# Kernel optimization log

Hardware: AMD Instinct MI355X
Metric: run time of the kernel (lower is better)

## Reference

```python
import jax, jax.numpy as jnp
import numpy as np

B, H, W, C = 4, 64, 64, 1280
NH = 16          # num heads
HD = C // NH     # 80 features per head
WS = 14          # window size
REL = 2 * WS - 1 # 27 relative-position entries per axis
EPS = 1e-6


def setup_inputs() -> dict:
    key = jax.random.key(0)
    ks = jax.random.split(key, 16)
    s = 0.02
    return {
        "imagelike_bhwc": jax.random.normal(ks[0], (B, H, W, C), jnp.float32),
        "ln1_g": jnp.ones((C,), jnp.float32),
        "ln1_b": jnp.zeros((C,), jnp.float32),
        "qkv_w": jax.random.normal(ks[1], (C, 3 * C), jnp.float32) * s,
        "qkv_b": jnp.zeros((3 * C,), jnp.float32),
        "proj_w": jax.random.normal(ks[2], (C, C), jnp.float32) * s,
        "proj_b": jnp.zeros((C,), jnp.float32),
        "rel_pos_h": jax.random.normal(ks[3], (REL, HD), jnp.float32) * s,
        "rel_pos_w": jax.random.normal(ks[4], (REL, HD), jnp.float32) * s,
        "ln2_g": jnp.ones((C,), jnp.float32),
        "ln2_b": jnp.zeros((C,), jnp.float32),
        "mlp_w1": jax.random.normal(ks[5], (C, 4 * C), jnp.float32) * s,
        "mlp_b1": jnp.zeros((4 * C,), jnp.float32),
        "mlp_w2": jax.random.normal(ks[6], (4 * C, C), jnp.float32) * s,
        "mlp_b2": jnp.zeros((C,), jnp.float32),
    }


def _layernorm(t, g, b):
    mu = jnp.mean(t, axis=-1, keepdims=True)
    var = jnp.var(t, axis=-1, keepdims=True)
    return (t - mu) * jax.lax.rsqrt(var + EPS) * g + b


def reference(imagelike_bhwc, ln1_g, ln1_b, qkv_w, qkv_b, proj_w, proj_b,
              rel_pos_h, rel_pos_w, ln2_g, ln2_b, mlp_w1, mlp_b1, mlp_w2, mlp_b2):
    x = imagelike_bhwc
    b, h, w, c = x.shape
    hd = c // NH
    scale = hd ** -0.5
    # --- image -> windows (pad to multiple of WS) ---
    hp, wp = (-h) % WS, (-w) % WS
    xp = jnp.pad(x, ((0, 0), (0, hp), (0, wp), (0, 0)))
    Hp, Wp = h + hp, w + wp
    ny, nx = Hp // WS, Wp // WS
    win = xp.reshape(b, ny, WS, nx, WS, c).transpose(0, 1, 3, 2, 4, 5)
    win = win.reshape(b * ny * nx, WS, WS, c)      # (Bw, S, S, C)
    Bw, N = win.shape[0], WS * WS
    # --- pre-attention layernorm + qkv ---
    t = _layernorm(win, ln1_g, ln1_b)
    qkv = t.reshape(Bw, N, c) @ qkv_w + qkv_b      # (Bw, N, 3C)
    qkv = qkv.reshape(Bw, N, 3, NH, hd).transpose(2, 0, 3, 1, 4)  # (3,Bw,NH,N,hd)
    q, k, v = qkv[0], qkv[1], qkv[2]
    # --- scores + decomposed relative position bias ---
    attn = jnp.einsum('bhqd,bhkd->bhqk', q * scale, k)            # (Bw,NH,N,N)
    idx = jnp.arange(WS)[:, None] - jnp.arange(WS)[None, :] + (WS - 1)
    Rh = rel_pos_h[idx]                                           # (WS,WS,hd)
    Rw = rel_pos_w[idx]                                           # (WS,WS,hd)
    qr = q.reshape(Bw, NH, WS, WS, hd)
    bias_h = jnp.einsum('bnyxd,ykd->bnyxk', qr, Rh)               # (Bw,NH,WS,WS,WS)
    bias_w = jnp.einsum('bnyxd,xkd->bnyxk', qr, Rw)
    bias = (bias_h[..., :, None] + bias_w[..., None, :]).reshape(Bw, NH, N, N)
    attn = jax.nn.softmax(attn + bias, axis=-1)
    out = jnp.einsum('bhqk,bhkd->bhqd', attn, v)                  # (Bw,NH,N,hd)
    out = out.transpose(0, 2, 1, 3).reshape(Bw, WS, WS, c)
    out = out @ proj_w + proj_b
    attn_out = out + win                                          # residual 1
    # --- MLP ---
    t2 = _layernorm(attn_out, ln2_g, ln2_b)
    mlp = jax.nn.gelu(t2 @ mlp_w1 + mlp_b1, approximate=False) @ mlp_w2 + mlp_b2
    out = mlp + attn_out                                          # residual 2
    # --- windows -> image (remove padding) ---
    img = out.reshape(b, ny, nx, WS, WS, c).transpose(0, 1, 3, 2, 4, 5)
    img = img.reshape(b, Hp, Wp, c)
    return img[:, :h, :w, :]
```

## Files before the change

### kernel.cpp

```cpp
#include <hip/hip_runtime.h>

typedef __attribute__((ext_vector_type(8))) short short8;
typedef __attribute__((ext_vector_type(4))) float f32x4;

#define GLBP(p) ((const __attribute__((address_space(1))) void*)(p))
#define LDSP(p) ((__attribute__((address_space(3))) void*)(p))

__device__ __forceinline__ float bf2f(unsigned short u) {
  return __uint_as_float(((unsigned int)u) << 16);
}
__device__ __forceinline__ unsigned short f2bf(float f) {
  unsigned int u = __float_as_uint(f);
  u += 0x7fff + ((u >> 16) & 1);
  return (unsigned short)(u >> 16);
}

__device__ __forceinline__ void tok2pix(int gt, int& b, int& py, int& px) {
  int w = gt / 196, t = gt - w * 196;
  b = w / 25;
  int wr = w - b * 25;
  int wy = wr / 5, wx = wr - wy * 5;
  int ty = t / 14;
  py = wy * 14 + ty;
  px = wx * 14 + (t - ty * 14);
}

__global__ void k_transpose(const float* __restrict__ W, unsigned short* __restrict__ Wt,
                            int K, int N) {
  __shared__ float tile[32][33];
  int tx = threadIdx.x, ty = threadIdx.y;
  int n0 = blockIdx.x * 32, k0 = blockIdx.y * 32;
#pragma unroll
  for (int i = 0; i < 4; ++i)
    tile[ty + 8 * i][tx] = W[(size_t)(k0 + ty + 8 * i) * N + n0 + tx];
  __syncthreads();
#pragma unroll
  for (int i = 0; i < 4; ++i)
    Wt[(size_t)(n0 + ty + 8 * i) * K + k0 + tx] = f2bf(tile[tx][ty + 8 * i]);
}

__global__ __launch_bounds__(256) void k_ln1(const float* __restrict__ x,
                                             const float* __restrict__ g,
                                             const float* __restrict__ be,
                                             unsigned short* __restrict__ A1,
                                             int w0, int ctok) {
  int m = blockIdx.x, tid = threadIdx.x;
  int b, py, px;
  tok2pix(w0 * 196 + m, b, py, px);
  bool valid = (m < ctok) && (py < 64) && (px < 64);
  const float* row = x + ((size_t)((b * 64 + py) * 64 + px)) * 1280;
  float v[5];
#pragma unroll
  for (int i = 0; i < 5; ++i) v[i] = valid ? row[tid + 256 * i] : 0.f;
  float s = 0.f, ss = 0.f;
#pragma unroll
  for (int i = 0; i < 5; ++i) { s += v[i]; ss += v[i] * v[i]; }
#pragma unroll
  for (int o = 32; o > 0; o >>= 1) { s += __shfl_down(s, o); ss += __shfl_down(ss, o); }
  __shared__ float rs[8];
  int wid = tid >> 6, lane = tid & 63;
  if (lane == 0) { rs[wid] = s; rs[wid + 4] = ss; }
  __syncthreads();
  s = rs[0] + rs[1] + rs[2] + rs[3];
  ss = rs[4] + rs[5] + rs[6] + rs[7];
  float mu = s * (1.f / 1280.f);
  float var = ss * (1.f / 1280.f) - mu * mu;
  float rinv = rsqrtf(var + 1e-6f);
  unsigned short* o1 = A1 + (size_t)m * 1280;
#pragma unroll
  for (int i = 0; i < 5; ++i) {
    int c = tid + 256 * i;
    o1[c] = f2bf((v[i] - mu) * rinv * g[c] + be[c]);
  }
}

__global__ __launch_bounds__(256) void k_ln2(const unsigned short* __restrict__ AT,
                                             const float* __restrict__ g,
                                             const float* __restrict__ be,
                                             unsigned short* __restrict__ A2) {
  int m = blockIdx.x, tid = threadIdx.x;
  const unsigned short* row = AT + (size_t)m * 1280;
  float v[5];
#pragma unroll
  for (int i = 0; i < 5; ++i) v[i] = bf2f(row[tid + 256 * i]);
  float s = 0.f, ss = 0.f;
#pragma unroll
  for (int i = 0; i < 5; ++i) { s += v[i]; ss += v[i] * v[i]; }
#pragma unroll
  for (int o = 32; o > 0; o >>= 1) { s += __shfl_down(s, o); ss += __shfl_down(ss, o); }
  __shared__ float rs[8];
  int wid = tid >> 6, lane = tid & 63;
  if (lane == 0) { rs[wid] = s; rs[wid + 4] = ss; }
  __syncthreads();
  s = rs[0] + rs[1] + rs[2] + rs[3];
  ss = rs[4] + rs[5] + rs[6] + rs[7];
  float mu = s * (1.f / 1280.f);
  float var = ss * (1.f / 1280.f) - mu * mu;
  float rinv = rsqrtf(var + 1e-6f);
  unsigned short* o1 = A2 + (size_t)m * 1280;
#pragma unroll
  for (int i = 0; i < 5; ++i) {
    int c = tid + 256 * i;
    o1[c] = f2bf((v[i] - mu) * rinv * g[c] + be[c]);
  }
}

template <int EPI>
__global__ __launch_bounds__(512, 2) void k_gemm256(const unsigned short* __restrict__ A,
                                                    const unsigned short* __restrict__ Bt,
                                                    int K, int N, int gx,
                                                    const float* __restrict__ bias,
                                                    void* __restrict__ outp,
                                                    const float* __restrict__ xres,
                                                    const unsigned short* __restrict__ attnres,
                                                    int w0, int ctok) {
  __shared__ __align__(16) char smem[131072];
  int tid = threadIdx.x;
  int w = tid >> 6, lane = tid & 63;
  int nwg = gridDim.x, bid = blockIdx.x;
  int q = nwg >> 3, r = nwg & 7;
  int xcd = bid & 7, loc = bid >> 3;
  int wg = (xcd < r ? xcd * (q + 1) : r * (q + 1) + (xcd - r) * q) + loc;
  int bx = wg % gx, by = wg / gx;
  int mBase = by * 256, nBase = bx * 256;
  int wr = w >> 2, wc = w & 3;
  int la = lane & 15, lg = lane >> 4;

  int rS = w * 16 + (lane >> 2);
  int kbyte = (((lane & 3) ^ ((lane >> 3) & 3)) << 4);
  const char* Ab = (const char*)A;
  const char* Bb = (const char*)Bt;
  const char* pa0 = Ab + ((size_t)(mBase + rS) * K) * 2 + kbyte;
  const char* pa1 = Ab + ((size_t)(mBase + 128 + rS) * K) * 2 + kbyte;
  const char* pb0 = Bb + ((size_t)(nBase + rS) * K) * 2 + kbyte;
  const char* pb1 = Bb + ((size_t)(nBase + 128 + rS) * K) * 2 + kbyte;
  int ldsw = w * 1024;

  auto STAGE = [&](int t) {
    int b = (t & 3) * 32768;
    size_t ko = (size_t)t * 64;
    __builtin_amdgcn_global_load_lds(GLBP(pa0 + ko), LDSP(smem + b + ldsw), 16, 0, 0);
    __builtin_amdgcn_global_load_lds(GLBP(pa1 + ko), LDSP(smem + b + 8192 + ldsw), 16, 0, 0);
    __builtin_amdgcn_global_load_lds(GLBP(pb0 + ko), LDSP(smem + b + 16384 + ldsw), 16, 0, 0);
    __builtin_amdgcn_global_load_lds(GLBP(pb1 + ko), LDSP(smem + b + 24576 + ldsw), 16, 0, 0);
  };

  int swz = ((lg ^ ((la >> 1) & 3)) << 4);
  int offA[8], offB[4];
#pragma unroll
  for (int m = 0; m < 8; ++m) offA[m] = (wr * 128 + m * 16 + la) * 64 + swz;
#pragma unroll
  for (int n = 0; n < 4; ++n) offB[n] = (wc * 64 + n * 16 + la) * 64 + swz;

  const f32x4 z4 = {0.f, 0.f, 0.f, 0.f};
  f32x4 acc[8][4];
#pragma unroll
  for (int m = 0; m < 8; ++m)
#pragma unroll
    for (int n = 0; n < 4; ++n) acc[m][n] = z4;

  int NT = K >> 5;
  STAGE(0);
  STAGE(1);
  STAGE(2);
  for (int t = 0; t < NT; ++t) {
    if (t + 2 < NT)
      asm volatile("s_waitcnt vmcnt(8)" ::: "memory");
    else if (t + 1 < NT)
      asm volatile("s_waitcnt vmcnt(4)" ::: "memory");
    else
      asm volatile("s_waitcnt vmcnt(0)" ::: "memory");
    __builtin_amdgcn_s_barrier();
    __builtin_amdgcn_sched_barrier(0);
    if (t + 3 < NT) STAGE(t + 3);
    const char* buf = (const char*)smem + (t & 3) * 32768;
    short8 af[8], bfr[4];
#pragma unroll
    for (int m = 0; m < 8; ++m) af[m] = *(const short8*)(buf + offA[m]);
#pragma unroll
    for (int n = 0; n < 4; ++n) bfr[n] = *(const short8*)(buf + 16384 + offB[n]);
    __builtin_amdgcn_s_setprio(1);
#pragma unroll
    for (int m = 0; m < 8; ++m)
#pragma unroll
      for (int n = 0; n < 4; ++n)
        acc[m][n] = __builtin_amdgcn_mfma_f32_16x16x32_bf16(af[m], bfr[n], acc[m][n], 0, 0, 0);
    __builtin_amdgcn_s_setprio(0);
  }

#pragma unroll
  for (int m = 0; m < 8; ++m) {
#pragma unroll
    for (int n = 0; n < 4; ++n) {
      int col = nBase + wc * 64 + n * 16 + la;
      float bcol = bias[col];
#pragma unroll
      for (int j = 0; j < 4; ++j) {
        int row = mBase + wr * 128 + m * 16 + lg * 4 + j;
        float v = acc[m][n][j] + bcol;
        if (EPI == 0) {
          ((unsigned short*)outp)[(size_t)row * N + col] = f2bf(v);
        } else if (EPI == 2) {
          float gg = 0.5f * v * (1.f + erff(v * 0.70710678118654752f));
          ((unsigned short*)outp)[(size_t)row * N + col] = f2bf(gg);
        } else if (EPI == 1) {
          if (row < ctok) {
            int b, py, px;
            tok2pix(w0 * 196 + row, b, py, px);
            float wv = (py < 64 && px < 64)
                           ? xres[((size_t)((b * 64 + py) * 64 + px)) * 1280 + col]
                           : 0.f;
            ((unsigned short*)outp)[(size_t)row * 1280 + col] = f2bf(v + wv);
          }
        } else {
          if (row < ctok) {
            int b, py, px;
            tok2pix(w0 * 196 + row, b, py, px);
            if (py < 64 && px < 64)
              ((float*)outp)[((size_t)((b * 64 + py) * 64 + px)) * 1280 + col] =
                  v + bf2f(attnres[(size_t)row * 1280 + col]);
          }
        }
      }
    }
  }
}

__global__ __launch_bounds__(256) void k_relbias(const unsigned short* __restrict__ qkv,
                                                 const float* __restrict__ rph,
                                                 const float* __restrict__ rpw,
                                                 float* __restrict__ B) {
  int wh = blockIdx.x;
  int w = wh >> 4, nh = wh & 15;
  const unsigned short* qb = qkv + (size_t)w * 196 * 3840 + nh * 80;
  for (int id = threadIdx.x; id < 196 * 28; id += 256) {
    int t = id / 28, which = id - t * 28;
    int y = t / 14, xx = t - y * 14;
    const float* R = (which < 14) ? (rph + (size_t)(y - which + 13) * 80)
                                  : (rpw + (size_t)(xx - (which - 14) + 13) * 80);
    const unsigned short* q = qb + (size_t)t * 3840;
    float acc = 0.f;
#pragma unroll
    for (int d8 = 0; d8 < 10; ++d8) {
      short8 qv = *(const short8*)(q + d8 * 8);
      const float4* Rv = (const float4*)(R + d8 * 8);
      float4 ra = Rv[0], rb = Rv[1];
      acc += bf2f((unsigned short)qv[0]) * ra.x + bf2f((unsigned short)qv[1]) * ra.y +
             bf2f((unsigned short)qv[2]) * ra.z + bf2f((unsigned short)qv[3]) * ra.w +
             bf2f((unsigned short)qv[4]) * rb.x + bf2f((unsigned short)qv[5]) * rb.y +
             bf2f((unsigned short)qv[6]) * rb.z + bf2f((unsigned short)qv[7]) * rb.w;
    }
    B[(size_t)wh * (196 * 28) + id] = acc;
  }
}

__global__ __launch_bounds__(256) void k_attn(const unsigned short* __restrict__ qkv,
                                              const float* __restrict__ Bias,
                                              unsigned short* __restrict__ AO) {
  __shared__ unsigned short Qs[208 * 96];
  __shared__ unsigned short Ks[208 * 96];
  __shared__ unsigned short Vt[80 * 224];
  __shared__ unsigned short Ps[4][16 * 224];
  int wh = blockIdx.x;
  int w = wh >> 4, nh = wh & 15;
  int tid = threadIdx.x, wid = tid >> 6, lane = tid & 63;
  const unsigned short* base = qkv + (size_t)w * 196 * 3840 + nh * 80;
  short8 z8 = {0, 0, 0, 0, 0, 0, 0, 0};
  for (int c = tid; c < 208 * 12; c += 256) {
    int t = c / 12, d8 = (c - t * 12) * 8;
    short8 qv = z8, kv = z8;
    if (t < 196 && d8 < 80) {
      const unsigned short* p = base + (size_t)t * 3840 + d8;
      qv = *(const short8*)(p);
      kv = *(const short8*)(p + 1280);
    }
    *(short8*)(Qs + t * 96 + d8) = qv;
    *(short8*)(Ks + t * 96 + d8) = kv;
  }
  for (int c = tid; c < 208 * 10; c += 256) {
    int t = c / 10, d8 = (c - t * 10) * 8;
    short8 vv = z8;
    if (t < 196) vv = *(const short8*)(base + (size_t)t * 3840 + 2560 + d8);
#pragma unroll
    for (int e = 0; e < 8; ++e) Vt[(d8 + e) * 224 + t] = (unsigned short)vv[e];
  }
  for (int i = tid; i < 80 * 16; i += 256) Vt[(i >> 4) * 224 + 208 + (i & 15)] = 0;
  __syncthreads();

  int la = lane & 15, lg = lane >> 4;
  const float scale = 0.111803398874989485f;
  const f32x4 z4 = {0.f, 0.f, 0.f, 0.f};
  unsigned short* P = Ps[wid];

  for (int rb = wid; rb < 13; rb += 4) {
    f32x4 s[13];
#pragma unroll
    for (int i = 0; i < 13; ++i) s[i] = z4;
#pragma unroll
    for (int kk = 0; kk < 3; ++kk) {
      short8 a = *(const short8*)(Qs + (rb * 16 + la) * 96 + kk * 32 + lg * 8);
#pragma unroll
      for (int ni = 0; ni < 13; ++ni) {
        short8 bb = *(const short8*)(Ks + (ni * 16 + la) * 96 + kk * 32 + lg * 8);
        s[ni] = __builtin_amdgcn_mfma_f32_16x16x32_bf16(a, bb, s[ni], 0, 0, 0);
      }
    }
#pragma unroll
    for (int j = 0; j < 4; ++j) {
      int rloc = lg * 4 + j;
      int t = rb * 16 + rloc;
      float v[13];
      float mx = -3e30f;
#pragma unroll
      for (int ci = 0; ci < 13; ++ci) {
        int key = ci * 16 + la;
        float val = s[ci][j] * scale;
        if (key < 196 && t < 196) {
          const float* Bp = Bias + ((size_t)wh * 196 + t) * 28;
          int ky = key / 14, kx = key - ky * 14;
          val += Bp[ky] + Bp[14 + kx];
        }
        if (key >= 196) val = -3e30f;
        v[ci] = val;
        mx = fmaxf(mx, val);
      }
#pragma unroll
      for (int o = 1; o < 16; o <<= 1) mx = fmaxf(mx, __shfl_xor(mx, o));
      float sum = 0.f;
#pragma unroll
      for (int ci = 0; ci < 13; ++ci) {
        float e = __expf(v[ci] - mx);
        v[ci] = e;
        sum += e;
      }
#pragma unroll
      for (int o = 1; o < 16; o <<= 1) sum += __shfl_xor(sum, o);
      float inv = 1.f / sum;
#pragma unroll
      for (int ci = 0; ci < 13; ++ci) P[rloc * 224 + ci * 16 + la] = f2bf(v[ci] * inv);
      P[rloc * 224 + 208 + la] = 0;
    }
    f32x4 o5[5];
#pragma unroll
    for (int i = 0; i < 5; ++i) o5[i] = z4;
#pragma unroll
    for (int kc = 0; kc < 7; ++kc) {
      short8 a = *(const short8*)(P + la * 224 + kc * 32 + lg * 8);
#pragma unroll
      for (int ni = 0; ni < 5; ++ni) {
        short8 bb = *(const short8*)(Vt + (ni * 16 + la) * 224 + kc * 32 + lg * 8);
        o5[ni] = __builtin_amdgcn_mfma_f32_16x16x32_bf16(a, bb, o5[ni], 0, 0, 0);
      }
    }
#pragma unroll
    for (int ni = 0; ni < 5; ++ni)
#pragma unroll
      for (int j = 0; j < 4; ++j) {
        int t = rb * 16 + lg * 4 + j;
        if (t < 196)
          AO[((size_t)w * 196 + t) * 1280 + nh * 80 + ni * 16 + la] = f2bf(o5[ni][j]);
      }
  }
}

extern "C" void kernel_launch(void* const* d_in, const int* in_sizes, int n_in,
                              void* d_out, int out_size, void* d_ws, size_t ws_size,
                              hipStream_t stream) {
  const float* x = (const float*)d_in[0];
  const float* ln1g = (const float*)d_in[1];
  const float* ln1b = (const float*)d_in[2];
  const float* qkvw = (const float*)d_in[3];
  const float* qkvb = (const float*)d_in[4];
  const float* projw = (const float*)d_in[5];
  const float* projb = (const float*)d_in[6];
  const float* rph = (const float*)d_in[7];
  const float* rpw = (const float*)d_in[8];
  const float* ln2g = (const float*)d_in[9];
  const float* ln2b = (const float*)d_in[10];
  const float* w1 = (const float*)d_in[11];
  const float* b1 = (const float*)d_in[12];
  const float* w2 = (const float*)d_in[13];
  const float* b2 = (const float*)d_in[14];
  float* out = (float*)d_out;

  const size_t woff = (3840ull * 1280 + 1280ull * 1280 + 5120ull * 1280 + 1280ull * 5120) * 2;
  const int NWopts[7] = {100, 50, 25, 10, 5, 2, 1};
  int NW = 0, Mb = 0;
  for (int i = 0; i < 7; ++i) {
    int nw = NWopts[i];
    int mb = ((nw * 196 + 255) / 256) * 256;
    size_t tot = woff + (size_t)mb * 2560  + (size_t)mb * 7680  +
                 (size_t)mb * 2560  + (size_t)nw * 16 * 196 * 28 * 4  +
                 (size_t)mb * 2560 ;
    if (tot <= ws_size) { NW = nw; Mb = mb; break; }
  }
  if (!NW) return;

  char* p = (char*)d_ws;
  unsigned short* qkvwT = (unsigned short*)p; p += 3840ull * 1280 * 2;
  unsigned short* projwT = (unsigned short*)p; p += 1280ull * 1280 * 2;
  unsigned short* w1T = (unsigned short*)p; p += 5120ull * 1280 * 2;
  unsigned short* w2T = (unsigned short*)p; p += 1280ull * 5120 * 2;
  unsigned short* A1 = (unsigned short*)p; p += (size_t)Mb * 2560;
  unsigned short* QKV = (unsigned short*)p; p += (size_t)Mb * 7680;
  unsigned short* AO = (unsigned short*)p; p += (size_t)Mb * 2560;
  float* BIAS = (float*)p; p += (size_t)NW * 16 * 196 * 28 * 4;
  unsigned short* ATTN = (unsigned short*)p;
  unsigned short* Hb = QKV;
  unsigned short* A2 = A1;

  k_transpose<<<dim3(120, 40), dim3(32, 8), 0, stream>>>(qkvw, qkvwT, 1280, 3840);
  k_transpose<<<dim3(40, 40), dim3(32, 8), 0, stream>>>(projw, projwT, 1280, 1280);
  k_transpose<<<dim3(160, 40), dim3(32, 8), 0, stream>>>(w1, w1T, 1280, 5120);
  k_transpose<<<dim3(40, 160), dim3(32, 8), 0, stream>>>(w2, w2T, 5120, 1280);

  int gy = Mb / 256;
  int nchunks = (100 + NW - 1) / NW;
  for (int c = 0; c < nchunks; ++c) {
    int w0 = c * NW;
    int cw = (100 - w0 < NW) ? (100 - w0) : NW;
    int ctok = cw * 196;
    k_ln1<<<Mb, 256, 0, stream>>>(x, ln1g, ln1b, A1, w0, ctok);
    k_gemm256<0><<<15 * gy, 512, 0, stream>>>(A1, qkvwT, 1280, 3840, 15, qkvb, (void*)QKV,
                                              nullptr, nullptr, 0, 0);
    k_relbias<<<cw * 16, 256, 0, stream>>>(QKV, rph, rpw, BIAS);
    k_attn<<<cw * 16, 256, 0, stream>>>(QKV, BIAS, AO);
    k_gemm256<1><<<5 * gy, 512, 0, stream>>>(AO, projwT, 1280, 1280, 5, projb, (void*)ATTN,
                                             x, nullptr, w0, ctok);
    k_ln2<<<Mb, 256, 0, stream>>>(ATTN, ln2g, ln2b, A2);
    k_gemm256<2><<<20 * gy, 512, 0, stream>>>(A2, w1T, 1280, 5120, 20, b1, (void*)Hb,
                                              nullptr, nullptr, 0, 0);
    k_gemm256<3><<<5 * gy, 512, 0, stream>>>(Hb, w2T, 5120, 1280, 5, b2, (void*)out,
                                             nullptr, ATTN, w0, ctok);
  }
}
```

Measured before the change: 1.869 ms.

## Split GEMM inner loop into two halves and restructure attention kernel

```diff
diff --git a/kernel.cpp b/kernel.cpp
--- a/kernel.cpp
+++ b/kernel.cpp
@@ -164,24 +164,36 @@
   STAGE(1);
   STAGE(2);
   for (int t = 0; t < NT; ++t) {
-    if (t + 2 < NT)
+    int rem = NT - 1 - t;
+    if (rem >= 2)
       asm volatile("s_waitcnt vmcnt(8)" ::: "memory");
-    else if (t + 1 < NT)
+    else if (rem == 1)
       asm volatile("s_waitcnt vmcnt(4)" ::: "memory");
     else
       asm volatile("s_waitcnt vmcnt(0)" ::: "memory");
     __builtin_amdgcn_s_barrier();
     __builtin_amdgcn_sched_barrier(0);
-    if (t + 3 < NT) STAGE(t + 3);
     const char* buf = (const char*)smem + (t & 3) * 32768;
     short8 af[8], bfr[4];
 #pragma unroll
-    for (int m = 0; m < 8; ++m) af[m] = *(const short8*)(buf + offA[m]);
+    for (int m = 0; m < 4; ++m) af[m] = *(const short8*)(buf + offA[m]);
 #pragma unroll
     for (int n = 0; n < 4; ++n) bfr[n] = *(const short8*)(buf + 16384 + offB[n]);
+    if (t + 3 < NT) STAGE(t + 3);
     __builtin_amdgcn_s_setprio(1);
 #pragma unroll
-    for (int m = 0; m < 8; ++m)
+    for (int m = 0; m < 4; ++m)
+#pragma unroll
+      for (int n = 0; n < 4; ++n)
+        acc[m][n] = __builtin_amdgcn_mfma_f32_16x16x32_bf16(af[m], bfr[n], acc[m][n], 0, 0, 0);
+    __builtin_amdgcn_s_setprio(0);
+    __builtin_amdgcn_s_barrier();
+    __builtin_amdgcn_sched_barrier(0);
+#pragma unroll
+    for (int m = 4; m < 8; ++m) af[m] = *(const short8*)(buf + offA[m]);
+    __builtin_amdgcn_s_setprio(1);
+#pragma unroll
+    for (int m = 4; m < 8; ++m)
 #pragma unroll
       for (int n = 0; n < 4; ++n)
         acc[m][n] = __builtin_amdgcn_mfma_f32_16x16x32_bf16(af[m], bfr[n], acc[m][n], 0, 0, 0);
@@ -229,7 +241,7 @@
 __global__ __launch_bounds__(256) void k_relbias(const unsigned short* __restrict__ qkv,
                                                  const float* __restrict__ rph,
                                                  const float* __restrict__ rpw,
-                                                 float* __restrict__ B) {
+                                                 unsigned short* __restrict__ B) {
   int wh = blockIdx.x;
   int w = wh >> 4, nh = wh & 15;
   const unsigned short* qb = qkv + (size_t)w * 196 * 3840 + nh * 80;
@@ -250,76 +262,87 @@
              bf2f((unsigned short)qv[4]) * rb.x + bf2f((unsigned short)qv[5]) * rb.y +
              bf2f((unsigned short)qv[6]) * rb.z + bf2f((unsigned short)qv[7]) * rb.w;
     }
-    B[(size_t)wh * (196 * 28) + id] = acc;
-  }
-}
-
-__global__ __launch_bounds__(256) void k_attn(const unsigned short* __restrict__ qkv,
-                                              const float* __restrict__ Bias,
+    B[(size_t)wh * (196 * 28) + id] = f2bf(acc);
+  }
+}
+
+__global__ __launch_bounds__(512) void k_attn(const unsigned short* __restrict__ qkv,
+                                              const unsigned short* __restrict__ Bias,
                                               unsigned short* __restrict__ AO) {
-  __shared__ unsigned short Qs[208 * 96];
-  __shared__ unsigned short Ks[208 * 96];
-  __shared__ unsigned short Vt[80 * 224];
-  __shared__ unsigned short Ps[4][16 * 224];
+  __shared__ unsigned short Ks[208 * 104];
+  __shared__ unsigned short Vt[80 * 248];
+  __shared__ unsigned short Ps[8][16 * 248];
+  __shared__ unsigned short Bls[196 * 28];
   int wh = blockIdx.x;
   int w = wh >> 4, nh = wh & 15;
   int tid = threadIdx.x, wid = tid >> 6, lane = tid & 63;
+  int la = lane & 15, lg = lane >> 4;
   const unsigned short* base = qkv + (size_t)w * 196 * 3840 + nh * 80;
-  short8 z8 = {0, 0, 0, 0, 0, 0, 0, 0};
-  for (int c = tid; c < 208 * 12; c += 256) {
-    int t = c / 12, d8 = (c - t * 12) * 8;
-    short8 qv = z8, kv = z8;
-    if (t < 196 && d8 < 80) {
-      const unsigned short* p = base + (size_t)t * 3840 + d8;
-      qv = *(const short8*)(p);
-      kv = *(const short8*)(p + 1280);
-    }
-    *(short8*)(Qs + t * 96 + d8) = qv;
-    *(short8*)(Ks + t * 96 + d8) = kv;
-  }
-  for (int c = tid; c < 208 * 10; c += 256) {
-    int t = c / 10, d8 = (c - t * 10) * 8;
-    short8 vv = z8;
-    if (t < 196) vv = *(const short8*)(base + (size_t)t * 3840 + 2560 + d8);
-#pragma unroll
-    for (int e = 0; e < 8; ++e) Vt[(d8 + e) * 224 + t] = (unsigned short)vv[e];
-  }
-  for (int i = tid; i < 80 * 16; i += 256) Vt[(i >> 4) * 224 + 208 + (i & 15)] = 0;
+  const short8 z8 = {0, 0, 0, 0, 0, 0, 0, 0};
+
+  for (int c = tid; c < 208 * 13; c += 512) {
+    int t = c / 13, seg = c - t * 13;
+    short8 kv = z8;
+    if (t < 196 && seg < 10) kv = *(const short8*)(base + (size_t)t * 3840 + 1280 + seg * 8);
+    *(short8*)(Ks + t * 104 + seg * 8) = kv;
+  }
+  for (int c = tid; c < 28 * 80; c += 512) {
+    int d = c % 80, tb = c / 80;
+    short8 pk;
+#pragma unroll
+    for (int e = 0; e < 8; ++e) {
+      int t = tb * 8 + e;
+      pk[e] = (t < 196) ? (short)base[(size_t)t * 3840 + 2560 + d] : (short)0;
+    }
+    *(short8*)(Vt + d * 248 + tb * 8) = pk;
+  }
+  for (int i = tid; i < 196 * 28; i += 512) Bls[i] = Bias[(size_t)wh * (196 * 28) + i];
   __syncthreads();
 
-  int la = lane & 15, lg = lane >> 4;
+  int kyv[13], kxv[13];
+#pragma unroll
+  for (int ci = 0; ci < 13; ++ci) {
+    int key = ci * 16 + la;
+    kyv[ci] = key / 14;
+    kxv[ci] = key - kyv[ci] * 14;
+  }
+
   const float scale = 0.111803398874989485f;
   const f32x4 z4 = {0.f, 0.f, 0.f, 0.f};
   unsigned short* P = Ps[wid];
 
-  for (int rb = wid; rb < 13; rb += 4) {
+  auto process = [&](int rb) {
+    short8 qa[3];
+#pragma unroll
+    for (int kk = 0; kk < 3; ++kk) {
+      int t = rb * 16 + la;
+      int d = kk * 32 + lg * 8;
+      qa[kk] = (t < 196 && d < 80) ? *(const short8*)(base + (size_t)t * 3840 + d) : z8;
+    }
     f32x4 s[13];
 #pragma unroll
     for (int i = 0; i < 13; ++i) s[i] = z4;
 #pragma unroll
     for (int kk = 0; kk < 3; ++kk) {
-      short8 a = *(const short8*)(Qs + (rb * 16 + la) * 96 + kk * 32 + lg * 8);
 #pragma unroll
       for (int ni = 0; ni < 13; ++ni) {
-        short8 bb = *(const short8*)(Ks + (ni * 16 + la) * 96 + kk * 32 + lg * 8);
-        s[ni] = __builtin_amdgcn_mfma_f32_16x16x32_bf16(a, bb, s[ni], 0, 0, 0);
+        short8 bb = *(const short8*)(Ks + (ni * 16 + la) * 104 + kk * 32 + lg * 8);
+        s[ni] = __builtin_amdgcn_mfma_f32_16x16x32_bf16(qa[kk], bb, s[ni], 0, 0, 0);
       }
     }
 #pragma unroll
     for (int j = 0; j < 4; ++j) {
       int rloc = lg * 4 + j;
       int t = rb * 16 + rloc;
+      bool tval = t < 196;
+      const unsigned short* Bp = Bls + (tval ? t : 0) * 28;
       float v[13];
       float mx = -3e30f;
 #pragma unroll
       for (int ci = 0; ci < 13; ++ci) {
         int key = ci * 16 + la;
         float val = s[ci][j] * scale;
-        if (key < 196 && t < 196) {
-          const float* Bp = Bias + ((size_t)wh * 196 + t) * 28;
-          int ky = key / 14, kx = key - ky * 14;
-          val += Bp[ky] + Bp[14 + kx];
-        }
+        if (key < 196 && tval) val += bf2f(Bp[kyv[ci]]) + bf2f(Bp[14 + kxv[ci]]);
         if (key >= 196) val = -3e30f;
         v[ci] = val;
         mx = fmaxf(mx, val);
@@ -337,18 +360,18 @@
       for (int o = 1; o < 16; o <<= 1) sum += __shfl_xor(sum, o);
       float inv = 1.f / sum;
 #pragma unroll
-      for (int ci = 0; ci < 13; ++ci) P[rloc * 224 + ci * 16 + la] = f2bf(v[ci] * inv);
-      P[rloc * 224 + 208 + la] = 0;
+      for (int ci = 0; ci < 13; ++ci) P[rloc * 248 + ci * 16 + la] = f2bf(v[ci] * inv);
+      P[rloc * 248 + 208 + la] = 0;
     }
     f32x4 o5[5];
 #pragma unroll
     for (int i = 0; i < 5; ++i) o5[i] = z4;
 #pragma unroll
     for (int kc = 0; kc < 7; ++kc) {
-      short8 a = *(const short8*)(P + la * 224 + kc * 32 + lg * 8);
+      short8 a = *(const short8*)(P + la * 248 + kc * 32 + lg * 8);
 #pragma unroll
       for (int ni = 0; ni < 5; ++ni) {
-        short8 bb = *(const short8*)(Vt + (ni * 16 + la) * 224 + kc * 32 + lg * 8);
+        short8 bb = *(const short8*)(Vt + (ni * 16 + la) * 248 + kc * 32 + lg * 8);
         o5[ni] = __builtin_amdgcn_mfma_f32_16x16x32_bf16(a, bb, o5[ni], 0, 0, 0);
       }
     }
@@ -360,7 +383,10 @@
         if (t < 196)
           AO[((size_t)w * 196 + t) * 1280 + nh * 80 + ni * 16 + la] = f2bf(o5[ni][j]);
       }
-  }
+  };
+
+  process(wid);
+  if (wid < 5) process(wid + 8);
 }
 
 extern "C" void kernel_launch(void* const* d_in, const int* in_sizes, int n_in,
@@ -390,7 +416,7 @@
     int nw = NWopts[i];
     int mb = ((nw * 196 + 255) / 256) * 256;
     size_t tot = woff + (size_t)mb * 2560  + (size_t)mb * 7680  +
-                 (size_t)mb * 2560  + (size_t)nw * 16 * 196 * 28 * 4  +
+                 (size_t)mb * 2560  + (size_t)nw * 16 * 196 * 28 * 2  +
                  (size_t)mb * 2560 ;
     if (tot <= ws_size) { NW = nw; Mb = mb; break; }
   }
@@ -404,7 +430,7 @@
   unsigned short* A1 = (unsigned short*)p; p += (size_t)Mb * 2560;
   unsigned short* QKV = (unsigned short*)p; p += (size_t)Mb * 7680;
   unsigned short* AO = (unsigned short*)p; p += (size_t)Mb * 2560;
-  float* BIAS = (float*)p; p += (size_t)NW * 16 * 196 * 28 * 4;
+  unsigned short* BIAS = (unsigned short*)p; p += (size_t)NW * 16 * 196 * 28 * 2;
   unsigned short* ATTN = (unsigned short*)p;
   unsigned short* Hb = QKV;
   unsigned short* A2 = A1;
@@ -424,7 +450,7 @@
     k_gemm256<0><<<15 * gy, 512, 0, stream>>>(A1, qkvwT, 1280, 3840, 15, qkvb, (void*)QKV,
                                               nullptr, nullptr, 0, 0);
     k_relbias<<<cw * 16, 256, 0, stream>>>(QKV, rph, rpw, BIAS);
-    k_attn<<<cw * 16, 256, 0, stream>>>(QKV, BIAS, AO);
+    k_attn<<<cw * 16, 512, 0, stream>>>(QKV, BIAS, AO);
     k_gemm256<1><<<5 * gy, 512, 0, stream>>>(AO, projwT, 1280, 1280, 5, projb, (void*)ATTN,
                                              x, nullptr, w0, ctok);
     k_ln2<<<Mb, 256, 0, stream>>>(ATTN, ln2g, ln2b, A2);
```

Result: faster. 1.730 ms (-7.4%).
